# Kernel optimization log

Measured on AMD Instinct MI355X. Metric: run time of the kernel, lower is better.

Reference implementation:

```python
import jax, jax.numpy as jnp
import numpy as np

N, F, H, C = 50000, 128, 4, 32   # nodes, in_channels, heads, hidden_channels
E, R, DE = 800000, 8, 64         # edges, num_relations, edge_dim


def setup_inputs() -> dict:
    key = jax.random.key(0)
    ks = jax.random.split(key, 10)
    x = jax.random.normal(ks[0], (N, F), dtype=jnp.float32)
    edge_index = jax.random.randint(ks[1], (2, E), 0, N, dtype=jnp.int64)
    edge_type = jax.random.randint(ks[2], (E,), 0, R, dtype=jnp.int64)
    s_in = 1.0 / np.sqrt(F)
    s_e = 1.0 / np.sqrt(DE)
    edge_emb = jax.random.normal(ks[3], (R, DE), dtype=jnp.float32)
    Wq = jax.random.normal(ks[4], (F, H * C), dtype=jnp.float32) * s_in
    Wk = jax.random.normal(ks[5], (F, H * C), dtype=jnp.float32) * s_in
    Wv = jax.random.normal(ks[6], (F, H * C), dtype=jnp.float32) * s_in
    We = jax.random.normal(ks[7], (DE, H * C), dtype=jnp.float32) * s_e
    Wskip = jax.random.normal(ks[8], (F, H * C), dtype=jnp.float32) * s_in
    return {"x": x, "edge_index": edge_index, "edge_type": edge_type,
            "edge_emb": edge_emb, "Wq": Wq, "Wk": Wk, "Wv": Wv,
            "We": We, "Wskip": Wskip}


def reference(x, edge_index, edge_type, edge_emb, Wq, Wk, Wv, We, Wskip):
    # TransformerConv (PyG) with edge embeddings, concat heads, root skip, no bias.
    src, dst = edge_index[0], edge_index[1]
    q = (x @ Wq).reshape(N, H, C)
    k = (x @ Wk).reshape(N, H, C)
    v = (x @ Wv).reshape(N, H, C)
    e = (edge_emb[edge_type] @ We).reshape(E, H, C)      # per-edge relation emb
    kj = k[src] + e                                       # [E,H,C]
    logits = (q[dst] * kj).sum(-1) / jnp.sqrt(jnp.float32(C))  # [E,H]
    # segment softmax over incoming edges of each target node
    m = jax.ops.segment_max(logits, dst, num_segments=N)  # [N,H]
    m = jnp.where(jnp.isfinite(m), m, jnp.float32(0.0))
    ex = jnp.exp(logits - m[dst])
    denom = jax.ops.segment_sum(ex, dst, num_segments=N)  # [N,H]
    alpha = ex / (denom[dst] + 1e-16)                     # [E,H]
    msg = (v[src] + e) * alpha[:, :, None]                # [E,H,C]
    out = jax.ops.segment_sum(msg, dst, num_segments=N).reshape(N, H * C)
    return out + x @ Wskip
```

## Files before the change

kernel.cpp:

```cpp
#include <hip/hip_runtime.h>
#include <hip/hip_bf16.h>

#define NN 50000
#define FF 128
#define NH 4
#define CH 32
#define HC 128
#define NE 800000
#define NR 8
#define DEDIM 64
#define PBLK 391
#define QKB 625
#define MTILES 3125
#define CAP 48

typedef __hip_bfloat16 bf16;
typedef __attribute__((ext_vector_type(8))) short short8;
typedef __attribute__((ext_vector_type(4))) float f32x4;

__device__ __forceinline__ float bflo(unsigned u) { return __uint_as_float(u << 16); }
__device__ __forceinline__ float bfhi(unsigned u) { return __uint_as_float(u & 0xFFFF0000u); }

__device__ __forceinline__ unsigned short f2bf(float f) {
  unsigned u = __float_as_uint(f);
  unsigned r = (u + 0x7FFFu + ((u >> 16) & 1u)) >> 16;
  return (unsigned short)r;
}
__device__ __forceinline__ unsigned pack2bf(float lo, float hi) {
  return (unsigned)f2bf(lo) | ((unsigned)f2bf(hi) << 16);
}

template <int ISBF>
__device__ __forceinline__ float ldf(const void* p, size_t i) {
  if (ISBF) return __bfloat162float(((const bf16*)p)[i]);
  return ((const float*)p)[i];
}

__global__ __launch_bounds__(256) void k_wt(const unsigned* __restrict__ xw,
    const void* __restrict__ Wq, const void* __restrict__ Ws,
    const void* __restrict__ Wk, const void* __restrict__ Wv,
    unsigned short* __restrict__ wtr, int* __restrict__ hist) {
  unsigned ex = (xw[threadIdx.x & 63] >> 7) & 0xFFu;
  unsigned long long bb = __ballot(ex < 90u || ex > 140u);
  int isbf = (bb == 0ULL);
  int i = blockIdx.x * 256 + threadIdx.x;
  int m = i >> 14, n = (i >> 7) & 127, k = i & 127;
  const void* W = (m == 0) ? Wq : (m == 1) ? Ws : (m == 2) ? Wk : Wv;
  wtr[i] = isbf ? ((const unsigned short*)W)[k * HC + n]
                : f2bf(((const float*)W)[k * HC + n]);
  if (i < NN) hist[i] = 0;
}

template <int ISBF>
__device__ __forceinline__ void qkvs4_body(const void* __restrict__ x,
    const unsigned short* __restrict__ wtr,
    unsigned short* __restrict__ qb, unsigned* __restrict__ kvb,
    void* __restrict__ out, unsigned char* __restrict__ est, int mc) {
  const int tid  = threadIdx.x;
  const int lane = tid & 63;
  const int wv   = tid >> 6;
  const int quad = lane >> 4;
  const int lr   = lane & 15;
  short8 bf[4][2][4];
#pragma unroll
  for (int m = 0; m < 4; ++m)
#pragma unroll
    for (int t = 0; t < 2; ++t) {
      int ncol = wv * 32 + t * 16 + lr;
#pragma unroll
      for (int kb = 0; kb < 4; ++kb)
        bf[m][t][kb] = *(const short8*)&wtr[(m * HC + ncol) * FF + kb * 32 + quad * 8];
    }
  unsigned short* qs  = (unsigned short*)est;
  unsigned short* sbs = (unsigned short*)(est + 4096);
  float*          sfs = (float*)(est + 4096);
  unsigned*       kvs = (unsigned*)est;
  const unsigned short* xu = (const unsigned short*)x;
  const float* xf = (const float*)x;
  short8 lda[4];
  float4 raw[8];
  {
    size_t off = (size_t)(mc * 16 + lr) * FF + quad * 8;
    if (ISBF) {
#pragma unroll
      for (int kb = 0; kb < 4; ++kb) lda[kb] = *(const short8*)(xu + off + kb * 32);
    } else {
#pragma unroll
      for (int kb = 0; kb < 4; ++kb) {
        raw[2 * kb]     = *(const float4*)(xf + off + kb * 32);
        raw[2 * kb + 1] = *(const float4*)(xf + off + kb * 32 + 4);
      }
    }
  }
  for (int mt = mc; mt < MTILES; mt += QKB) {
    int m0 = mt * 16;
    short8 cur[4];
    if (ISBF) {
#pragma unroll
      for (int kb = 0; kb < 4; ++kb) cur[kb] = lda[kb];
    } else {
#pragma unroll
      for (int kb = 0; kb < 4; ++kb) {
        float4 a = raw[2 * kb], b = raw[2 * kb + 1];
        short8 o;
        o[0] = (short)f2bf(a.x); o[1] = (short)f2bf(a.y);
        o[2] = (short)f2bf(a.z); o[3] = (short)f2bf(a.w);
        o[4] = (short)f2bf(b.x); o[5] = (short)f2bf(b.y);
        o[6] = (short)f2bf(b.z); o[7] = (short)f2bf(b.w);
        cur[kb] = o;
      }
    }
    int mtn = mt + QKB;
    if (mtn < MTILES) {
      size_t off = (size_t)(mtn * 16 + lr) * FF + quad * 8;
      if (ISBF) {
#pragma unroll
        for (int kb = 0; kb < 4; ++kb) lda[kb] = *(const short8*)(xu + off + kb * 32);
      } else {
#pragma unroll
        for (int kb = 0; kb < 4; ++kb) {
          raw[2 * kb]     = *(const float4*)(xf + off + kb * 32);
          raw[2 * kb + 1] = *(const float4*)(xf + off + kb * 32 + 4);
        }
      }
    }
    f32x4 acc[4][2];
#pragma unroll
    for (int m = 0; m < 4; ++m)
#pragma unroll
      for (int t = 0; t < 2; ++t) acc[m][t] = {0.f, 0.f, 0.f, 0.f};
#pragma unroll
    for (int kb = 0; kb < 4; ++kb)
#pragma unroll
      for (int m = 0; m < 4; ++m) {
        acc[m][0] = __builtin_amdgcn_mfma_f32_16x16x32_bf16(cur[kb], bf[m][0][kb], acc[m][0], 0, 0, 0);
        acc[m][1] = __builtin_amdgcn_mfma_f32_16x16x32_bf16(cur[kb], bf[m][1][kb], acc[m][1], 0, 0, 0);
      }
#pragma unroll
    for (int t = 0; t < 2; ++t)
#pragma unroll
      for (int r = 0; r < 4; ++r) {
        int li = (quad * 4 + r) * HC + wv * 32 + t * 16 + lr;
        qs[li] = f2bf(acc[0][t][r]);
        if (ISBF) sbs[li] = f2bf(acc[1][t][r]);
        else      sfs[li] = acc[1][t][r];
      }
    __syncthreads();
    {
      int row = tid >> 4, seg = tid & 15;
      *(uint4*)(qb + (size_t)(m0 + row) * HC + seg * 8) = ((const uint4*)qs)[tid];
      if (ISBF) {
        *(uint4*)((unsigned short*)out + (size_t)(m0 + row) * HC + seg * 8) =
            ((const uint4*)sbs)[tid];
      } else {
#pragma unroll
        for (int s = 0; s < 2; ++s) {
          int idx = s * 256 + tid, rw = idx >> 5, sg = idx & 31;
          *(uint4*)((float*)out + (size_t)(m0 + rw) * HC + sg * 4) =
              ((const uint4*)sfs)[idx];
        }
      }
    }
    __syncthreads();
#pragma unroll
    for (int t = 0; t < 2; ++t)
#pragma unroll
      for (int r = 0; r < 4; ++r) {
        int li = (quad * 4 + r) * HC + wv * 32 + t * 16 + lr;
        kvs[li] = pack2bf(acc[2][t][r], acc[3][t][r]);
      }
    __syncthreads();
#pragma unroll
    for (int s = 0; s < 2; ++s) {
      int idx = s * 256 + tid, rw = idx >> 5, sg = idx & 31;
      *(uint4*)(kvb + (size_t)(m0 + rw) * HC + sg * 4) = ((const uint4*)kvs)[idx];
    }
    __syncthreads();
  }
}

__global__ __launch_bounds__(256) void k_fused(const unsigned* __restrict__ xw,
    const int* __restrict__ eidx32, const void* __restrict__ etype,
    const void* __restrict__ emb, const void* __restrict__ We,
    const unsigned short* __restrict__ wtr,
    int* __restrict__ flag, int* __restrict__ hist, float* __restrict__ ee,
    int* __restrict__ bucket,
    unsigned short* __restrict__ qb, unsigned* __restrict__ kvb,
    void* __restrict__ out) {
  __shared__ __align__(16) unsigned char shm[12288];
  if (blockIdx.x < PBLK) {
    unsigned long long b = __ballot(eidx32[2 * (threadIdx.x & 63) + 1] != 0);
    int is64 = (b == 0ULL);
    int e0 = (blockIdx.x * 256 + threadIdx.x) * 8;
    if (e0 >= NE) return;
    int src[8], dst[8], et[8];
    if (is64) {
      const int4* p4 = (const int4*)eidx32;
      const int4* t4 = (const int4*)etype;
#pragma unroll
      for (int j = 0; j < 4; ++j) {
        int4 a = p4[(e0 >> 1) + j];
        int4 c = p4[((NE + e0) >> 1) + j];
        int4 t0 = t4[(e0 >> 1) + j];
        src[2 * j] = a.x;  src[2 * j + 1] = a.z;
        dst[2 * j] = c.x;  dst[2 * j + 1] = c.z;
        et[2 * j]  = t0.x; et[2 * j + 1]  = t0.z;
      }
    } else {
      const int4* p4 = (const int4*)eidx32;
      const int4* t4 = (const int4*)etype;
#pragma unroll
      for (int j = 0; j < 2; ++j) {
        int4 a = p4[(e0 >> 2) + j];
        int4 c = p4[((NE + e0) >> 2) + j];
        int4 t0 = t4[(e0 >> 2) + j];
        src[4 * j] = a.x; src[4 * j + 1] = a.y; src[4 * j + 2] = a.z; src[4 * j + 3] = a.w;
        dst[4 * j] = c.x; dst[4 * j + 1] = c.y; dst[4 * j + 2] = c.z; dst[4 * j + 3] = c.w;
        et[4 * j]  = t0.x; et[4 * j + 1] = t0.y; et[4 * j + 2] = t0.z; et[4 * j + 3] = t0.w;
      }
    }
    int rank[8];
#pragma unroll
    for (int u = 0; u < 8; ++u) {
      int dd = min(max(dst[u], 0), NN - 1);
      dst[u] = dd;
      rank[u] = atomicAdd(&hist[dd], 1);
    }
#pragma unroll
    for (int u = 0; u < 8; ++u) {
      int s  = min(max(src[u], 0), NN - 1);
      int tt = min(max(et[u], 0), NR - 1);
      int rk = min(rank[u], CAP - 1);
      bucket[dst[u] * CAP + rk] = (s << 3) | tt;
    }
    return;
  }
  if (blockIdx.x < PBLK + QKB) {
    unsigned ex = (xw[threadIdx.x & 63] >> 7) & 0xFFu;
    unsigned long long bb = __ballot(ex < 90u || ex > 140u);
    int isbf = (bb == 0ULL);
    int mc = blockIdx.x - PBLK;
    if (isbf) qkvs4_body<1>(xw, wtr, qb, kvb, out, shm, mc);
    else      qkvs4_body<0>(xw, wtr, qb, kvb, out, shm, mc);
    return;
  }
  float* es = (float*)shm;
  __shared__ int nzIdx, badBf;
  if (threadIdx.x == 0) { nzIdx = 0; badBf = 0; }
  __syncthreads();
  if (threadIdx.x < 128) {
    if (eidx32[2 * threadIdx.x + 1] != 0) atomicAdd(&nzIdx, 1);
    unsigned e = (xw[threadIdx.x] >> 7) & 0xFFu;
    if (e < 90u || e > 140u) atomicAdd(&badBf, 1);
  }
  __syncthreads();
  const int isbf = (badBf == 0);
  if (threadIdx.x == 0) { flag[0] = (nzIdx == 0); flag[1] = isbf; }
  for (int i = threadIdx.x; i < NR * DEDIM; i += 256)
    es[i] = isbf ? ldf<1>(emb, i) : ldf<0>(emb, i);
  __syncthreads();
  for (int o = threadIdx.x; o < NR * HC; o += 256) {
    int r = o >> 7, j = o & 127;
    float acc = 0.f;
    if (isbf) { for (int d = 0; d < DEDIM; ++d) acc += es[r * DEDIM + d] * ldf<1>(We, d * HC + j); }
    else      { for (int d = 0; d < DEDIM; ++d) acc += es[r * DEDIM + d] * ldf<0>(We, d * HC + j); }
    ee[o] = acc;
  }
}

__global__ __launch_bounds__(256) void k_gather(const int* __restrict__ hist,
    const int* __restrict__ bucket, const unsigned short* __restrict__ qb,
    const unsigned* __restrict__ kvb, const float* __restrict__ ee,
    const int* __restrict__ flag, void* __restrict__ out) {
  int n = blockIdx.x * 4 + (threadIdx.x >> 6);
  int l = threadIdx.x & 63;
  int t = l >> 5;
  int w = l & 31;
  int j0 = ((w >> 3) << 5) + ((w & 7) << 2);
  int end = min(__builtin_amdgcn_readfirstlane(hist[n]), CAP);
  const int* row = bucket + n * CAP;
  uint2 qw = *(const uint2*)(qb + (size_t)n * HC + j0);
  float q0 = bflo(qw.x), q1 = bfhi(qw.x), q2 = bflo(qw.y), q3 = bfhi(qw.y);
  const float sc = 0.17677669529663687f;
  float dn = 0.f, a0 = 0.f, a1 = 0.f, a2 = 0.f, a3 = 0.f;
  int p = 0;
  for (; p + 16 <= end; p += 16) {
    int se[8]; uint4 kv[8]; float4 ev[8];
#pragma unroll
    for (int u = 0; u < 8; ++u) se[u] = row[p + 2 * u + t];
#pragma unroll
    for (int u = 0; u < 8; ++u)
      kv[u] = *(const uint4*)(kvb + (size_t)(se[u] >> 3) * HC + j0);
#pragma unroll
    for (int u = 0; u < 8; ++u)
      ev[u] = *(const float4*)(ee + ((se[u] & 7) << 7) + j0);
#pragma unroll
    for (int u = 0; u < 8; ++u) {
      float pp = q0 * (bflo(kv[u].x) + ev[u].x) + q1 * (bflo(kv[u].y) + ev[u].y)
               + q2 * (bflo(kv[u].z) + ev[u].z) + q3 * (bflo(kv[u].w) + ev[u].w);
      pp += __shfl_xor(pp, 1);
      pp += __shfl_xor(pp, 2);
      pp += __shfl_xor(pp, 4);
      float xx = __expf(pp * sc);
      dn += xx;
      a0 += (bfhi(kv[u].x) + ev[u].x) * xx;
      a1 += (bfhi(kv[u].y) + ev[u].y) * xx;
      a2 += (bfhi(kv[u].z) + ev[u].z) * xx;
      a3 += (bfhi(kv[u].w) + ev[u].w) * xx;
    }
  }
  if (p + 8 <= end) {
    int se[4]; uint4 kv[4]; float4 ev[4];
#pragma unroll
    for (int u = 0; u < 4; ++u) se[u] = row[p + 2 * u + t];
#pragma unroll
    for (int u = 0; u < 4; ++u)
      kv[u] = *(const uint4*)(kvb + (size_t)(se[u] >> 3) * HC + j0);
#pragma unroll
    for (int u = 0; u < 4; ++u)
      ev[u] = *(const float4*)(ee + ((se[u] & 7) << 7) + j0);
#pragma unroll
    for (int u = 0; u < 4; ++u) {
      float pp = q0 * (bflo(kv[u].x) + ev[u].x) + q1 * (bflo(kv[u].y) + ev[u].y)
               + q2 * (bflo(kv[u].z) + ev[u].z) + q3 * (bflo(kv[u].w) + ev[u].w);
      pp += __shfl_xor(pp, 1);
      pp += __shfl_xor(pp, 2);
      pp += __shfl_xor(pp, 4);
      float xx = __expf(pp * sc);
      dn += xx;
      a0 += (bfhi(kv[u].x) + ev[u].x) * xx;
      a1 += (bfhi(kv[u].y) + ev[u].y) * xx;
      a2 += (bfhi(kv[u].z) + ev[u].z) * xx;
      a3 += (bfhi(kv[u].w) + ev[u].w) * xx;
    }
    p += 8;
  }
  if (p < end) {
    int se[4]; bool ok[4]; uint4 kv[4]; float4 ev[4];
#pragma unroll
    for (int u = 0; u < 4; ++u) {
      int pe = p + 2 * u + t;
      ok[u] = pe < end;
      se[u] = row[ok[u] ? pe : 0];
    }
#pragma unroll
    for (int u = 0; u < 4; ++u)
      kv[u] = *(const uint4*)(kvb + (size_t)(se[u] >> 3) * HC + j0);
#pragma unroll
    for (int u = 0; u < 4; ++u)
      ev[u] = *(const float4*)(ee + ((se[u] & 7) << 7) + j0);
#pragma unroll
    for (int u = 0; u < 4; ++u) {
      float pp = q0 * (bflo(kv[u].x) + ev[u].x) + q1 * (bflo(kv[u].y) + ev[u].y)
               + q2 * (bflo(kv[u].z) + ev[u].z) + q3 * (bflo(kv[u].w) + ev[u].w);
      pp += __shfl_xor(pp, 1);
      pp += __shfl_xor(pp, 2);
      pp += __shfl_xor(pp, 4);
      float xx = ok[u] ? __expf(pp * sc) : 0.f;
      dn += xx;
      a0 += (bfhi(kv[u].x) + ev[u].x) * xx;
      a1 += (bfhi(kv[u].y) + ev[u].y) * xx;
      a2 += (bfhi(kv[u].z) + ev[u].z) * xx;
      a3 += (bfhi(kv[u].w) + ev[u].w) * xx;
    }
  }
  dn += __shfl_xor(dn, 32);
  a0 += __shfl_xor(a0, 32);
  a1 += __shfl_xor(a1, 32);
  a2 += __shfl_xor(a2, 32);
  a3 += __shfl_xor(a3, 32);
  if (t == 0) {
    float inv = 1.f / (dn + 1e-16f);
    size_t oi = (size_t)n * HC + j0;
    if (flag[1]) {
      uint2 sk = *(const uint2*)((const unsigned short*)out + oi);
      uint2 o;
      o.x = pack2bf(a0 * inv + bflo(sk.x), a1 * inv + bfhi(sk.x));
      o.y = pack2bf(a2 * inv + bflo(sk.y), a3 * inv + bfhi(sk.y));
      *(uint2*)((unsigned short*)out + oi) = o;
    } else {
      float4 sk = *(const float4*)((const float*)out + oi);
      float4 o = make_float4(a0 * inv + sk.x, a1 * inv + sk.y,
                             a2 * inv + sk.z, a3 * inv + sk.w);
      *(float4*)((float*)out + oi) = o;
    }
  }
}

extern "C" void kernel_launch(void* const* d_in, const int* in_sizes, int n_in,
                              void* d_out, int out_size, void* d_ws, size_t ws_size,
                              hipStream_t stream) {
  const void* x     = d_in[0];
  const void* eidx  = d_in[1];
  const void* etype = d_in[2];
  const void* emb   = d_in[3];
  const void* Wq    = d_in[4];
  const void* Wk    = d_in[5];
  const void* Wv    = d_in[6];
  const void* We    = d_in[7];
  const void* Ws    = d_in[8];

  float* base   = (float*)d_ws;
  int*   flag   = (int*)base;
  float* ee     = base + 16;
  unsigned short* wtr = (unsigned short*)(base + 1040);
  int*   hist   = (int*)(base + 33824);
  int*   bucket = (int*)(base + 83840);
  unsigned short* qb  = (unsigned short*)(base + 2483840);
  unsigned*       kvb = (unsigned*)(base + 5683840);

  k_wt    <<<256, 256, 0, stream>>>((const unsigned*)x, Wq, Ws, Wk, Wv,
                                    wtr, hist);
  k_fused <<<PBLK + QKB + 1, 256, 0, stream>>>((const unsigned*)x,
                                               (const int*)eidx, etype, emb, We,
                                               wtr, flag, hist, ee, bucket,
                                               qb, kvb, d_out);
  k_gather<<<NN / 4, 256, 0, stream>>>(hist, bucket, qb, kvb, ee, flag, d_out);
}
```

Measured before the change: 247.8 us.

## Coarsen edge bucketing, use lighter LDS barriers, shrink gather unroll

The bucketing blocks now each handle 32 edges per thread instead of 8, cutting that partition from 391 blocks to 98. The QKV projection replaces __syncthreads with a barrier that waits only on LDS/scalar counters, not outstanding global stores. The gather loop drops its 16-edge unrolled body and keeps only the 8-edge step, lowering register pressure at the cost of fewer loads in flight. Fewer bucketing blocks may reduce latency hiding of the atomics.

Result: faster. 213.3 us (-13.9%).

```diff
diff --git a/kernel.cpp b/kernel.cpp
--- a/kernel.cpp
+++ b/kernel.cpp
@@ -9,7 +9,7 @@
 #define NE 800000
 #define NR 8
 #define DEDIM 64
-#define PBLK 391
+#define PBLK 98
 #define QKB 625
 #define MTILES 3125
 #define CAP 48
@@ -28,6 +28,10 @@
 }
 __device__ __forceinline__ unsigned pack2bf(float lo, float hi) {
   return (unsigned)f2bf(lo) | ((unsigned)f2bf(hi) << 16);
+}
+
+__device__ __forceinline__ void ldsbar() {
+  asm volatile("s_waitcnt lgkmcnt(0)\n\ts_barrier" ::: "memory");
 }
 
 template <int ISBF>
@@ -145,7 +149,7 @@
         if (ISBF) sbs[li] = f2bf(acc[1][t][r]);
         else      sfs[li] = acc[1][t][r];
       }
-    __syncthreads();
+    ldsbar();
     {
       int row = tid >> 4, seg = tid & 15;
       *(uint4*)(qb + (size_t)(m0 + row) * HC + seg * 8) = ((const uint4*)qs)[tid];
@@ -161,7 +165,7 @@
         }
       }
     }
-    __syncthreads();
+    ldsbar();
 #pragma unroll
     for (int t = 0; t < 2; ++t)
 #pragma unroll
@@ -169,13 +173,13 @@
         int li = (quad * 4 + r) * HC + wv * 32 + t * 16 + lr;
         kvs[li] = pack2bf(acc[2][t][r], acc[3][t][r]);
       }
-    __syncthreads();
+    ldsbar();
 #pragma unroll
     for (int s = 0; s < 2; ++s) {
       int idx = s * 256 + tid, rw = idx >> 5, sg = idx & 31;
       *(uint4*)(kvb + (size_t)(m0 + rw) * HC + sg * 4) = ((const uint4*)kvs)[idx];
     }
-    __syncthreads();
+    ldsbar();
   }
 }
 
@@ -191,47 +195,51 @@
   if (blockIdx.x < PBLK) {
     unsigned long long b = __ballot(eidx32[2 * (threadIdx.x & 63) + 1] != 0);
     int is64 = (b == 0ULL);
-    int e0 = (blockIdx.x * 256 + threadIdx.x) * 8;
-    if (e0 >= NE) return;
-    int src[8], dst[8], et[8];
-    if (is64) {
-      const int4* p4 = (const int4*)eidx32;
-      const int4* t4 = (const int4*)etype;
-#pragma unroll
-      for (int j = 0; j < 4; ++j) {
-        int4 a = p4[(e0 >> 1) + j];
-        int4 c = p4[((NE + e0) >> 1) + j];
-        int4 t0 = t4[(e0 >> 1) + j];
-        src[2 * j] = a.x;  src[2 * j + 1] = a.z;
-        dst[2 * j] = c.x;  dst[2 * j + 1] = c.z;
-        et[2 * j]  = t0.x; et[2 * j + 1]  = t0.z;
-      }
-    } else {
-      const int4* p4 = (const int4*)eidx32;
-      const int4* t4 = (const int4*)etype;
-#pragma unroll
-      for (int j = 0; j < 2; ++j) {
-        int4 a = p4[(e0 >> 2) + j];
-        int4 c = p4[((NE + e0) >> 2) + j];
-        int4 t0 = t4[(e0 >> 2) + j];
-        src[4 * j] = a.x; src[4 * j + 1] = a.y; src[4 * j + 2] = a.z; src[4 * j + 3] = a.w;
-        dst[4 * j] = c.x; dst[4 * j + 1] = c.y; dst[4 * j + 2] = c.z; dst[4 * j + 3] = c.w;
-        et[4 * j]  = t0.x; et[4 * j + 1] = t0.y; et[4 * j + 2] = t0.z; et[4 * j + 3] = t0.w;
-      }
-    }
-    int rank[8];
-#pragma unroll
-    for (int u = 0; u < 8; ++u) {
-      int dd = min(max(dst[u], 0), NN - 1);
-      dst[u] = dd;
-      rank[u] = atomicAdd(&hist[dd], 1);
-    }
-#pragma unroll
-    for (int u = 0; u < 8; ++u) {
-      int s  = min(max(src[u], 0), NN - 1);
-      int tt = min(max(et[u], 0), NR - 1);
-      int rk = min(rank[u], CAP - 1);
-      bucket[dst[u] * CAP + rk] = (s << 3) | tt;
+    int ebase = (blockIdx.x * 256 + threadIdx.x) * 32;
+    if (ebase >= NE) return;
+#pragma unroll
+    for (int c = 0; c < 4; ++c) {
+      int e0 = ebase + c * 8;
+      int src[8], dst[8], et[8];
+      if (is64) {
+        const int4* p4 = (const int4*)eidx32;
+        const int4* t4 = (const int4*)etype;
+#pragma unroll
+        for (int j = 0; j < 4; ++j) {
+          int4 a = p4[(e0 >> 1) + j];
+          int4 cc = p4[((NE + e0) >> 1) + j];
+          int4 t0 = t4[(e0 >> 1) + j];
+          src[2 * j] = a.x;  src[2 * j + 1] = a.z;
+          dst[2 * j] = cc.x; dst[2 * j + 1] = cc.z;
+          et[2 * j]  = t0.x; et[2 * j + 1]  = t0.z;
+        }
+      } else {
+        const int4* p4 = (const int4*)eidx32;
+        const int4* t4 = (const int4*)etype;
+#pragma unroll
+        for (int j = 0; j < 2; ++j) {
+          int4 a = p4[(e0 >> 2) + j];
+          int4 cc = p4[((NE + e0) >> 2) + j];
+          int4 t0 = t4[(e0 >> 2) + j];
+          src[4 * j] = a.x; src[4 * j + 1] = a.y; src[4 * j + 2] = a.z; src[4 * j + 3] = a.w;
+          dst[4 * j] = cc.x; dst[4 * j + 1] = cc.y; dst[4 * j + 2] = cc.z; dst[4 * j + 3] = cc.w;
+          et[4 * j]  = t0.x; et[4 * j + 1] = t0.y; et[4 * j + 2] = t0.z; et[4 * j + 3] = t0.w;
+        }
+      }
+      int rank[8];
+#pragma unroll
+      for (int u = 0; u < 8; ++u) {
+        int dd = min(max(dst[u], 0), NN - 1);
+        dst[u] = dd;
+        rank[u] = atomicAdd(&hist[dd], 1);
+      }
+#pragma unroll
+      for (int u = 0; u < 8; ++u) {
+        int s  = min(max(src[u], 0), NN - 1);
+        int tt = min(max(et[u], 0), NR - 1);
+        int rk = min(rank[u], CAP - 1);
+        bucket[dst[u] * CAP + rk] = (s << 3) | tt;
+      }
     }
     return;
   }
@@ -284,32 +292,7 @@
   const float sc = 0.17677669529663687f;
   float dn = 0.f, a0 = 0.f, a1 = 0.f, a2 = 0.f, a3 = 0.f;
   int p = 0;
-  for (; p + 16 <= end; p += 16) {
-    int se[8]; uint4 kv[8]; float4 ev[8];
-#pragma unroll
-    for (int u = 0; u < 8; ++u) se[u] = row[p + 2 * u + t];
-#pragma unroll
-    for (int u = 0; u < 8; ++u)
-      kv[u] = *(const uint4*)(kvb + (size_t)(se[u] >> 3) * HC + j0);
-#pragma unroll
-    for (int u = 0; u < 8; ++u)
-      ev[u] = *(const float4*)(ee + ((se[u] & 7) << 7) + j0);
-#pragma unroll
-    for (int u = 0; u < 8; ++u) {
-      float pp = q0 * (bflo(kv[u].x) + ev[u].x) + q1 * (bflo(kv[u].y) + ev[u].y)
-               + q2 * (bflo(kv[u].z) + ev[u].z) + q3 * (bflo(kv[u].w) + ev[u].w);
-      pp += __shfl_xor(pp, 1);
-      pp += __shfl_xor(pp, 2);
-      pp += __shfl_xor(pp, 4);
-      float xx = __expf(pp * sc);
-      dn += xx;
-      a0 += (bfhi(kv[u].x) + ev[u].x) * xx;
-      a1 += (bfhi(kv[u].y) + ev[u].y) * xx;
-      a2 += (bfhi(kv[u].z) + ev[u].z) * xx;
-      a3 += (bfhi(kv[u].w) + ev[u].w) * xx;
-    }
-  }
-  if (p + 8 <= end) {
+  for (; p + 8 <= end; p += 8) {
     int se[4]; uint4 kv[4]; float4 ev[4];
 #pragma unroll
     for (int u = 0; u < 4; ++u) se[u] = row[p + 2 * u + t];
@@ -333,7 +316,6 @@
       a2 += (bfhi(kv[u].z) + ev[u].z) * xx;
       a3 += (bfhi(kv[u].w) + ev[u].w) * xx;
     }
-    p += 8;
   }
   if (p < end) {
     int se[4]; bool ok[4]; uint4 kv[4]; float4 ev[4];
```
